# Kernel optimization log

Hardware: AMD Instinct MI355X
Metric: run time of the kernel (lower is better)

Reference implementation:

```python
import jax, jax.numpy as jnp
import numpy as np

B, N, NIN, NH, NOUT = 32, 64, 256, 256, 2
E = N * (N - 1)
BN_EPS = 1e-5


def _xavier(k, fan_in, fan_out):
    return jax.random.normal(k, (fan_in, fan_out), jnp.float32) * np.sqrt(2.0 / (fan_in + fan_out))


def _mlp_params(key, n_in, n_hid, n_out):
    k1, k2 = jax.random.split(key)
    return {
        'w1': _xavier(k1, n_in, n_hid), 'b1': jnp.full((n_hid,), 0.1, jnp.float32),
        'w2': _xavier(k2, n_hid, n_out), 'b2': jnp.full((n_out,), 0.1, jnp.float32),
        'g': jnp.ones((n_out,), jnp.float32), 'beta': jnp.zeros((n_out,), jnp.float32),
    }


def setup_inputs() -> dict:
    key = jax.random.key(0)
    ks = jax.random.split(key, 7)
    inputs = jax.random.normal(ks[0], (B, N, NIN), jnp.float32)
    # fully-connected directed graph w/o self loops: edge e = (send i, recv j), i != j
    idx = np.array([(i, j) for i in range(N) for j in range(N) if i != j], dtype=np.int64)
    rel_send = np.zeros((E, N), np.float32)
    rel_rec = np.zeros((E, N), np.float32)
    rel_send[np.arange(E), idx[:, 0]] = 1.0
    rel_rec[np.arange(E), idx[:, 1]] = 1.0
    out = {'inputs': inputs, 'rel_rec': jnp.asarray(rel_rec), 'rel_send': jnp.asarray(rel_send)}
    for name, (ni, nh, no), k in [('mlp1', (NIN, NH, NH), ks[1]),
                                  ('mlp2', (2 * NH, NH, NH), ks[2]),
                                  ('mlp3', (NH, NH, NH), ks[3]),
                                  ('mlp4', (3 * NH, NH, NH), ks[4])]:
        p = _mlp_params(k, ni, nh, no)
        for pk, pv in p.items():
            out[f'{name}_{pk}'] = pv
    out['fc_w'] = _xavier(ks[5], NH, NOUT)
    out['fc_b'] = jnp.full((NOUT,), 0.1, jnp.float32)
    return out


def _mlp(x, w1, b1, w2, b2, g, beta):
    # Linear -> ELU -> Linear -> ELU -> BatchNorm1d (training-mode batch stats, biased var)
    h = jax.nn.elu(x @ w1 + b1)
    h = jax.nn.elu(h @ w2 + b2)
    mean = h.mean(axis=(0, 1))
    var = h.var(axis=(0, 1))
    return (h - mean) * jax.lax.rsqrt(var + BN_EPS) * g + beta


def reference(inputs, rel_rec, rel_send,
              mlp1_w1, mlp1_b1, mlp1_w2, mlp1_b2, mlp1_g, mlp1_beta,
              mlp2_w1, mlp2_b1, mlp2_w2, mlp2_b2, mlp2_g, mlp2_beta,
              mlp3_w1, mlp3_b1, mlp3_w2, mlp3_b2, mlp3_g, mlp3_beta,
              mlp4_w1, mlp4_b1, mlp4_w2, mlp4_b2, mlp4_g, mlp4_beta,
              fc_w, fc_b):
    x = _mlp(inputs, mlp1_w1, mlp1_b1, mlp1_w2, mlp1_b2, mlp1_g, mlp1_beta)  # [B,N,NH]
    # node2edge: gather sender/receiver node features per edge
    s = jnp.einsum('en,bnh->beh', rel_send, x)
    r = jnp.einsum('en,bnh->beh', rel_rec, x)
    x = jnp.concatenate([s, r], axis=-1)  # [B,E,2*NH]
    x = _mlp(x, mlp2_w1, mlp2_b1, mlp2_w2, mlp2_b2, mlp2_g, mlp2_beta)
    x_skip = x
    # edge2node: scatter-sum incoming edges per node, normalized by N
    inc = jnp.einsum('en,beh->bnh', rel_rec, x) / N
    x = _mlp(inc, mlp3_w1, mlp3_b1, mlp3_w2, mlp3_b2, mlp3_g, mlp3_beta)
    s = jnp.einsum('en,bnh->beh', rel_send, x)
    r = jnp.einsum('en,bnh->beh', rel_rec, x)
    x = jnp.concatenate([s, r, x_skip], axis=-1)  # [B,E,3*NH]
    x = _mlp(x, mlp4_w1, mlp4_b1, mlp4_w2, mlp4_b2, mlp4_g, mlp4_beta)
    return x @ fc_w + fc_b  # [B,E,NOUT]
```

## Files before the change

### kernel.cpp

```cpp
#include <hip/hip_runtime.h>

typedef __bf16 bf16_t;
typedef __bf16 bf16x8 __attribute__((ext_vector_type(8)));
typedef float  f32x4  __attribute__((ext_vector_type(4)));

#define NB    64
#define EB    4032
#define BATCH 32
#define H     256
#define M_EDGE (BATCH*EB)
#define M_NODE (BATCH*NB)
#define T2    4
#define BN_EPS 1e-5f

__device__ __forceinline__ void load_lds16(const void* g, void* l) {
    __builtin_amdgcn_global_load_lds(
        (const __attribute__((address_space(1))) unsigned int*)g,
        (__attribute__((address_space(3))) unsigned int*)l, 16, 0, 0);
}
__device__ __forceinline__ float elu(float v) { return v > 0.f ? v : __expf(v) - 1.f; }

template<bool AF32>
__global__ __launch_bounds__(256)
void fused_mlp(const void* __restrict__ A0v,
               const bf16_t* __restrict__ W1t, const float* __restrict__ b1,
               const bf16_t* __restrict__ W2t, const float* __restrict__ b2,
               bf16_t* __restrict__ out, float* __restrict__ stats)
{
    const int m0 = blockIdx.x * 64;
    const int tid = threadIdx.x, wave = tid >> 6, lane = tid & 63;
    const int l15 = lane & 15, quad = lane >> 4;
    const int row = tid >> 2;
    const int cx8 = (((tid & 3) ^ ((tid >> 3) & 3))) * 8;
    const int sl8 = (tid & 3) * 8;
    const int xq8 = (quad ^ ((l15 >> 1) & 3)) * 8;

    __shared__ bf16_t h1s[64 * 264];
    __shared__ bf16_t Bs[256 * 32];
    __shared__ float  sred[512];

    const bf16_t* A0 = (const bf16_t*)A0v;

    f32x4 acc1[4][4];
#pragma unroll
    for (int t = 0; t < 4; ++t)
#pragma unroll
        for (int u = 0; u < 4; ++u) acc1[t][u] = (f32x4){0.f, 0.f, 0.f, 0.f};

    for (int k0 = 0; k0 < 256; k0 += 32) {
        bf16_t* ldsA = h1s + wave * 512;
        if (AF32) {
            const float* af = (const float*)A0v + (size_t)(m0 + row) * 256 + k0 + cx8;
            float4 lo = *(const float4*)af;
            float4 hi = *(const float4*)(af + 4);
            bf16x8 v;
            v[0]=(bf16_t)lo.x; v[1]=(bf16_t)lo.y; v[2]=(bf16_t)lo.z; v[3]=(bf16_t)lo.w;
            v[4]=(bf16_t)hi.x; v[5]=(bf16_t)hi.y; v[6]=(bf16_t)hi.z; v[7]=(bf16_t)hi.w;
            *(bf16x8*)&h1s[row * 32 + sl8] = v;
        } else {
            load_lds16(A0 + (size_t)(m0 + row) * 256 + k0 + cx8, ldsA);
        }
#pragma unroll
        for (int p = 0; p < 4; ++p)
            load_lds16(W1t + (size_t)(p * 64 + row) * 256 + k0 + cx8,
                       Bs + (p * 256 + wave * 64) * 8);
        __syncthreads();
        bf16x8 afr[4], bfr[4];
#pragma unroll
        for (int t = 0; t < 4; ++t)
            afr[t] = *(const bf16x8*)&h1s[(t * 16 + l15) * 32 + xq8];
#pragma unroll
        for (int u = 0; u < 4; ++u)
            bfr[u] = *(const bf16x8*)&Bs[(wave * 64 + u * 16 + l15) * 32 + xq8];
#pragma unroll
        for (int t = 0; t < 4; ++t)
#pragma unroll
            for (int u = 0; u < 4; ++u)
                acc1[t][u] = __builtin_amdgcn_mfma_f32_16x16x32_bf16(afr[t], bfr[u], acc1[t][u], 0, 0, 0);
        __syncthreads();
    }

#pragma unroll
    for (int u = 0; u < 4; ++u) {
        int   col = wave * 64 + u * 16 + l15;
        float bv  = b1[col];
#pragma unroll
        for (int t = 0; t < 4; ++t)
#pragma unroll
            for (int r = 0; r < 4; ++r)
                h1s[(t * 16 + quad * 4 + r) * 264 + col] = (bf16_t)elu(acc1[t][u][r] + bv);
    }
    sred[tid] = 0.f; sred[256 + tid] = 0.f;
    __syncthreads();

    f32x4 acc2[4][4];
#pragma unroll
    for (int t = 0; t < 4; ++t)
#pragma unroll
        for (int u = 0; u < 4; ++u) acc2[t][u] = (f32x4){0.f, 0.f, 0.f, 0.f};

    for (int k0 = 0; k0 < 256; k0 += 32) {
#pragma unroll
        for (int p = 0; p < 4; ++p)
            load_lds16(W2t + (size_t)(p * 64 + row) * 256 + k0 + cx8,
                       Bs + (p * 256 + wave * 64) * 8);
        __syncthreads();
        bf16x8 afr[4], bfr[4];
#pragma unroll
        for (int t = 0; t < 4; ++t)
            afr[t] = *(const bf16x8*)&h1s[(t * 16 + l15) * 264 + k0 + quad * 8];
#pragma unroll
        for (int u = 0; u < 4; ++u)
            bfr[u] = *(const bf16x8*)&Bs[(wave * 64 + u * 16 + l15) * 32 + xq8];
#pragma unroll
        for (int t = 0; t < 4; ++t)
#pragma unroll
            for (int u = 0; u < 4; ++u)
                acc2[t][u] = __builtin_amdgcn_mfma_f32_16x16x32_bf16(afr[t], bfr[u], acc2[t][u], 0, 0, 0);
        __syncthreads();
    }

#pragma unroll
    for (int u = 0; u < 4; ++u) {
        int   col = wave * 64 + u * 16 + l15;
        float bv  = b2[col];
        float s = 0.f, q = 0.f;
#pragma unroll
        for (int t = 0; t < 4; ++t)
#pragma unroll
            for (int r = 0; r < 4; ++r) {
                float v = elu(acc2[t][u][r] + bv);
                h1s[(t * 16 + quad * 4 + r) * 264 + col] = (bf16_t)v;
                s += v; q += v * v;
            }
        s += __shfl_xor(s, 16); s += __shfl_xor(s, 32);
        q += __shfl_xor(q, 16); q += __shfl_xor(q, 32);
        if (quad == 0) { atomicAdd(&sred[col], s); atomicAdd(&sred[256 + col], q); }
    }
    __syncthreads();
#pragma unroll
    for (int p = 0; p < 8; ++p) {
        int idx = p * 256 + tid;
        int r = idx >> 5, ch = idx & 31;
        *(uint4*)&out[(size_t)(m0 + r) * H + ch * 8] = *(const uint4*)&h1s[r * 264 + ch * 8];
    }
    atomicAdd(&stats[tid],     sred[tid]);
    atomicAdd(&stats[H + tid], sred[256 + tid]);
}

__global__ __launch_bounds__(256)
void node_gemm(const bf16_t* __restrict__ A, const float* __restrict__ statsIn,
               const float* __restrict__ g, const float* __restrict__ beta, float Mcnt,
               const bf16_t* __restrict__ Wt, const float* __restrict__ bias,
               float* __restrict__ out)
{
    const int m0 = blockIdx.x * 64;
    const int nb = blockIdx.y * 256;
    const int tid = threadIdx.x, wave = tid >> 6, lane = tid & 63;
    const int l15 = lane & 15, quad = lane >> 4;
    const int row = tid >> 2;
    const int cx8 = (((tid & 3) ^ ((tid >> 3) & 3))) * 8;
    const int sl8 = (tid & 3) * 8;
    const int xq8 = (quad ^ ((l15 >> 1) & 3)) * 8;
    __shared__ bf16_t As[64 * 32];
    __shared__ bf16_t Bs[256 * 32];
    __shared__ float  ss[512];

    {
        float mean = statsIn[tid] / Mcnt;
        float var  = statsIn[256 + tid] / Mcnt - mean * mean;
        float scl  = g[tid] * rsqrtf(var + BN_EPS);
        ss[tid]       = scl;
        ss[256 + tid] = beta[tid] - mean * scl;
    }
    __syncthreads();

    f32x4 acc[4][4];
#pragma unroll
    for (int t = 0; t < 4; ++t)
#pragma unroll
        for (int u = 0; u < 4; ++u) acc[t][u] = (f32x4){0.f, 0.f, 0.f, 0.f};

    for (int k0 = 0; k0 < 256; k0 += 32) {
        {
            int kc = k0 + cx8;
            bf16x8 v = *(const bf16x8*)(A + (size_t)(m0 + row) * 256 + kc);
            bf16x8 w;
#pragma unroll
            for (int j = 0; j < 8; ++j)
                w[j] = (bf16_t)((float)v[j] * ss[kc + j] + ss[256 + kc + j]);
            *(bf16x8*)&As[row * 32 + sl8] = w;
        }
#pragma unroll
        for (int p = 0; p < 4; ++p)
            load_lds16(Wt + (size_t)(nb + p * 64 + row) * 256 + k0 + cx8,
                       Bs + (p * 256 + wave * 64) * 8);
        __syncthreads();
        bf16x8 afr[4], bfr[4];
#pragma unroll
        for (int t = 0; t < 4; ++t)
            afr[t] = *(const bf16x8*)&As[(t * 16 + l15) * 32 + xq8];
#pragma unroll
        for (int u = 0; u < 4; ++u)
            bfr[u] = *(const bf16x8*)&Bs[(wave * 64 + u * 16 + l15) * 32 + xq8];
#pragma unroll
        for (int t = 0; t < 4; ++t)
#pragma unroll
            for (int u = 0; u < 4; ++u)
                acc[t][u] = __builtin_amdgcn_mfma_f32_16x16x32_bf16(afr[t], bfr[u], acc[t][u], 0, 0, 0);
        __syncthreads();
    }
#pragma unroll
    for (int u = 0; u < 4; ++u) {
        int col = nb + wave * 64 + u * 16 + l15;
        float bv = bias[col];
#pragma unroll
        for (int t = 0; t < 4; ++t)
#pragma unroll
            for (int r = 0; r < 4; ++r)
                out[(size_t)(m0 + t * 16 + quad * 4 + r) * 512 + col] = acc[t][u][r] + bv;
    }
}

__global__ __launch_bounds__(256, 2)
void m2_kernel(const float* __restrict__ PQ, const bf16_t* __restrict__ W2t,
               const float* __restrict__ b2, bf16_t* __restrict__ out,
               float* __restrict__ stats)
{
    const int tile0 = blockIdx.x * T2;
    const int tid = threadIdx.x, wave = tid >> 6, lane = tid & 63;
    const int l15 = lane & 15, quad = lane >> 4;

    __shared__ bf16_t Abuf[2][64 * 264];
    __shared__ float  sred[512];

    bf16x8 Breg[32];
#pragma unroll
    for (int ks = 0; ks < 8; ++ks)
#pragma unroll
        for (int u = 0; u < 4; ++u) {
            int col = wave * 64 + u * 16 + l15;
            Breg[ks * 4 + u] = *(const bf16x8*)(W2t + (size_t)col * 256 + ks * 32 + quad * 8);
        }
    sred[tid] = 0.f; sred[256 + tid] = 0.f;

    auto computeA = [&](int t, int b) {
        int row = tid >> 2;
        int m = (tile0 + t) * 64 + row;
        int bb = m / EB, e = m - bb * EB;
        int sn = e / (NB - 1), rr = e - sn * (NB - 1);
        int rc = rr + (rr >= sn ? 1 : 0);
        const float* Prow = PQ + (size_t)(bb * NB + sn) * 512;
        const float* Qrow = PQ + (size_t)(bb * NB + rc) * 512 + 256;
        int c0 = (tid & 3) * 64;
#pragma unroll
        for (int j = 0; j < 8; ++j) {
            int c = c0 + j * 8;
            float4 p0 = *(const float4*)(Prow + c);
            float4 p1 = *(const float4*)(Prow + c + 4);
            float4 q0 = *(const float4*)(Qrow + c);
            float4 q1 = *(const float4*)(Qrow + c + 4);
            bf16x8 v;
            v[0]=(bf16_t)elu(p0.x+q0.x); v[1]=(bf16_t)elu(p0.y+q0.y);
            v[2]=(bf16_t)elu(p0.z+q0.z); v[3]=(bf16_t)elu(p0.w+q0.w);
            v[4]=(bf16_t)elu(p1.x+q1.x); v[5]=(bf16_t)elu(p1.y+q1.y);
            v[6]=(bf16_t)elu(p1.z+q1.z); v[7]=(bf16_t)elu(p1.w+q1.w);
            *(bf16x8*)&Abuf[b][row * 264 + c] = v;
        }
    };

    computeA(0, 0);
    __syncthreads();

    for (int t = 0; t < T2; ++t) {
        const int cur = t & 1, nxt = cur ^ 1;
        if (t + 1 < T2) computeA(t + 1, nxt);

        f32x4 acc[4][4];
#pragma unroll
        for (int a = 0; a < 4; ++a)
#pragma unroll
            for (int u = 0; u < 4; ++u) acc[a][u] = (f32x4){0.f, 0.f, 0.f, 0.f};
#pragma unroll
        for (int ks = 0; ks < 8; ++ks) {
            bf16x8 afr[4];
#pragma unroll
            for (int a = 0; a < 4; ++a)
                afr[a] = *(const bf16x8*)&Abuf[cur][(a * 16 + l15) * 264 + ks * 32 + quad * 8];
#pragma unroll
            for (int a = 0; a < 4; ++a)
#pragma unroll
                for (int u = 0; u < 4; ++u)
                    acc[a][u] = __builtin_amdgcn_mfma_f32_16x16x32_bf16(afr[a], Breg[ks * 4 + u], acc[a][u], 0, 0, 0);
        }
        __syncthreads();

#pragma unroll
        for (int u = 0; u < 4; ++u) {
            int   col = wave * 64 + u * 16 + l15;
            float bv  = b2[col];
            float s = 0.f, q = 0.f;
#pragma unroll
            for (int a = 0; a < 4; ++a)
#pragma unroll
                for (int r = 0; r < 4; ++r) {
                    float v = elu(acc[a][u][r] + bv);
                    Abuf[cur][(a * 16 + quad * 4 + r) * 264 + col] = (bf16_t)v;
                    s += v; q += v * v;
                }
            s += __shfl_xor(s, 16); s += __shfl_xor(s, 32);
            q += __shfl_xor(q, 16); q += __shfl_xor(q, 32);
            if (quad == 0) { atomicAdd(&sred[col], s); atomicAdd(&sred[256 + col], q); }
        }
        __syncthreads();

        size_t m0 = (size_t)(tile0 + t) * 64;
#pragma unroll
        for (int p = 0; p < 8; ++p) {
            int idx = p * 256 + tid;
            int r = idx >> 5, ch = idx & 31;
            *(uint4*)&out[(m0 + r) * H + ch * 8] = *(const uint4*)&Abuf[cur][r * 264 + ch * 8];
        }
        __syncthreads();
    }
    atomicAdd(&stats[tid],     sred[tid]);
    atomicAdd(&stats[H + tid], sred[256 + tid]);
}

__global__ __launch_bounds__(256, 3)
void m4_kernel(const bf16_t* __restrict__ h2, const bf16_t* __restrict__ Wskf,
               const float* __restrict__ RS, const bf16_t* __restrict__ W4f,
               const float* __restrict__ b2, bf16_t* __restrict__ out,
               float* __restrict__ stats)
{
    const int m0 = blockIdx.x * 64;
    const int tid = threadIdx.x, wave = tid >> 6, lane = tid & 63;
    const int l15 = lane & 15, quad = lane >> 4;
    const int row = tid >> 2;
    const int c0 = (tid & 3) * 64;

    __shared__ bf16_t h1s[64 * 264];
    __shared__ float  sred[512];

    sred[tid] = 0.f; sred[256 + tid] = 0.f;

    {
        const bf16_t* src = h2 + (size_t)(m0 + row) * 256;
#pragma unroll
        for (int j = 0; j < 8; ++j) {
            int c = c0 + j * 8;
            *(bf16x8*)&h1s[row * 264 + c] = *(const bf16x8*)(src + c);
        }
    }

    const bf16_t* WskW = Wskf + (size_t)wave * 16384;
    const bf16_t* W4W  = W4f  + (size_t)wave * 16384;

    bf16x8 bcur[4], bnxt[4];
#pragma unroll
    for (int u = 0; u < 4; ++u)
        bcur[u] = *(const bf16x8*)(WskW + u * 512 + lane * 8);
    __syncthreads();

    f32x4 acc[4][4];
#pragma unroll
    for (int a = 0; a < 4; ++a)
#pragma unroll
        for (int u = 0; u < 4; ++u) acc[a][u] = (f32x4){0.f, 0.f, 0.f, 0.f};

#pragma unroll
    for (int ks = 0; ks < 8; ++ks) {
        if (ks < 7) {
#pragma unroll
            for (int u = 0; u < 4; ++u)
                bnxt[u] = *(const bf16x8*)(WskW + (ks + 1) * 2048 + u * 512 + lane * 8);
        }
        bf16x8 afr[4];
#pragma unroll
        for (int a = 0; a < 4; ++a)
            afr[a] = *(const bf16x8*)&h1s[(a * 16 + l15) * 264 + ks * 32 + quad * 8];
#pragma unroll
        for (int a = 0; a < 4; ++a)
#pragma unroll
            for (int u = 0; u < 4; ++u)
                acc[a][u] = __builtin_amdgcn_mfma_f32_16x16x32_bf16(afr[a], bcur[u], acc[a][u], 0, 0, 0);
#pragma unroll
        for (int u = 0; u < 4; ++u) bcur[u] = bnxt[u];
    }

#pragma unroll
    for (int u = 0; u < 4; ++u)
        bcur[u] = *(const bf16x8*)(W4W + u * 512 + lane * 8);
    __syncthreads();

#pragma unroll
    for (int u = 0; u < 4; ++u) {
        int col = wave * 64 + u * 16 + l15;
#pragma unroll
        for (int a = 0; a < 4; ++a)
#pragma unroll
            for (int r = 0; r < 4; ++r)
                h1s[(a * 16 + quad * 4 + r) * 264 + col] = (bf16_t)acc[a][u][r];
    }
    __syncthreads();

    {
        int m = m0 + row;
        int bb = m / EB, e = m - bb * EB;
        int sn = e / (NB - 1), rr = e - sn * (NB - 1);
        int rc = rr + (rr >= sn ? 1 : 0);
        const float* Srow = RS + (size_t)(bb * NB + sn) * 512;
        const float* Rrow = RS + (size_t)(bb * NB + rc) * 512 + 256;
#pragma unroll
        for (int j = 0; j < 8; ++j) {
            int c = c0 + j * 8;
            bf16x8 h = *(const bf16x8*)&h1s[row * 264 + c];
            float4 s0 = *(const float4*)(Srow + c);
            float4 s1 = *(const float4*)(Srow + c + 4);
            float4 r0 = *(const float4*)(Rrow + c);
            float4 r1 = *(const float4*)(Rrow + c + 4);
            bf16x8 v;
            v[0]=(bf16_t)elu((float)h[0]+s0.x+r0.x); v[1]=(bf16_t)elu((float)h[1]+s0.y+r0.y);
            v[2]=(bf16_t)elu((float)h[2]+s0.z+r0.z); v[3]=(bf16_t)elu((float)h[3]+s0.w+r0.w);
            v[4]=(bf16_t)elu((float)h[4]+s1.x+r1.x); v[5]=(bf16_t)elu((float)h[5]+s1.y+r1.y);
            v[6]=(bf16_t)elu((float)h[6]+s1.z+r1.z); v[7]=(bf16_t)elu((float)h[7]+s1.w+r1.w);
            *(bf16x8*)&h1s[row * 264 + c] = v;
        }
    }
    __syncthreads();

#pragma unroll
    for (int a = 0; a < 4; ++a)
#pragma unroll
        for (int u = 0; u < 4; ++u) acc[a][u] = (f32x4){0.f, 0.f, 0.f, 0.f};
#pragma unroll
    for (int ks = 0; ks < 8; ++ks) {
        if (ks < 7) {
#pragma unroll
            for (int u = 0; u < 4; ++u)
                bnxt[u] = *(const bf16x8*)(W4W + (ks + 1) * 2048 + u * 512 + lane * 8);
        }
        bf16x8 afr[4];
#pragma unroll
        for (int a = 0; a < 4; ++a)
            afr[a] = *(const bf16x8*)&h1s[(a * 16 + l15) * 264 + ks * 32 + quad * 8];
#pragma unroll
        for (int a = 0; a < 4; ++a)
#pragma unroll
            for (int u = 0; u < 4; ++u)
                acc[a][u] = __builtin_amdgcn_mfma_f32_16x16x32_bf16(afr[a], bcur[u], acc[a][u], 0, 0, 0);
#pragma unroll
        for (int u = 0; u < 4; ++u) bcur[u] = bnxt[u];
    }
    __syncthreads();

#pragma unroll
    for (int u = 0; u < 4; ++u) {
        int   col = wave * 64 + u * 16 + l15;
        float bv  = b2[col];
        float s = 0.f, q = 0.f;
#pragma unroll
        for (int a = 0; a < 4; ++a)
#pragma unroll
            for (int r = 0; r < 4; ++r) {
                float v = elu(acc[a][u][r] + bv);
                h1s[(a * 16 + quad * 4 + r) * 264 + col] = (bf16_t)v;
                s += v; q += v * v;
            }
        s += __shfl_xor(s, 16); s += __shfl_xor(s, 32);
        q += __shfl_xor(q, 16); q += __shfl_xor(q, 32);
        if (quad == 0) { atomicAdd(&sred[col], s); atomicAdd(&sred[256 + col], q); }
    }
    __syncthreads();

#pragma unroll
    for (int p = 0; p < 8; ++p) {
        int idx = p * 256 + tid;
        int r = idx >> 5, ch = idx & 31;
        *(uint4*)&out[(size_t)(m0 + r) * H + ch * 8] = *(const uint4*)&h1s[r * 264 + ch * 8];
    }
    atomicAdd(&stats[tid],     sred[tid]);
    atomicAdd(&stats[H + tid], sred[256 + tid]);
}

__global__ void prep(const float* __restrict__ w1a, bf16_t* __restrict__ wt1a,
                     const float* __restrict__ w1b, bf16_t* __restrict__ wt1b,
                     const float* __restrict__ w2b, bf16_t* __restrict__ wt2b,
                     const float* __restrict__ w3a, bf16_t* __restrict__ wt3a,
                     const float* __restrict__ w3b, bf16_t* __restrict__ wt3b,
                     const float* __restrict__ w4b, bf16_t* __restrict__ wt4b,
                     const float* __restrict__ w2a, bf16_t* __restrict__ wtpq,
                     const float* __restrict__ w4a, bf16_t* __restrict__ wtrs,
                     const float* __restrict__ b2a, float* __restrict__ biasPQ,
                     float* __restrict__ stats)
{
    int blk = blockIdx.x, tid = threadIdx.x;
    if (blk < 1536) {
        int grp = blk >> 8, lb = blk & 255;
        int idx = lb * 256 + tid;
        int k = idx >> 8, n = idx & 255;
        if (grp == 5) {
            int wv = n >> 6, u = (n >> 4) & 3, l15 = n & 15;
            int ks = k >> 5, qd = (k >> 3) & 3, j = k & 7;
            wt4b[wv * 16384 + ks * 2048 + u * 512 + (qd * 16 + l15) * 8 + j] = (bf16_t)w4b[idx];
        } else {
            const float* w; bf16_t* wt;
            switch (grp) {
                case 0: w = w1a; wt = wt1a; break;
                case 1: w = w1b; wt = wt1b; break;
                case 2: w = w2b; wt = wt2b; break;
                case 3: w = w3a; wt = wt3a; break;
                default: w = w3b; wt = wt3b; break;
            }
            wt[n * 256 + k] = (bf16_t)w[idx];
        }
    } else if (blk < 2560) {
        int lb = blk - 1536;
        const float* w = (lb < 512) ? w2a : w4a;
        bf16_t* wt = (lb < 512) ? wtpq : wtrs;
        int c = lb & 511, k = tid;
        float v = (c < 256) ? w[k * 256 + c] : w[(256 + k) * 256 + (c - 256)];
        wt[c * 256 + k] = (bf16_t)v;
    } else if (blk == 2560) {
        biasPQ[tid] = b2a[tid];
        biasPQ[256 + tid] = 0.f;
    } else {
        for (int j = 0; j < 8; ++j) stats[j * 256 + tid] = 0.f;
    }
}

__global__ void prep2(const float* __restrict__ w4a, const float* __restrict__ stats2,
                      const float* __restrict__ g2, const float* __restrict__ be2,
                      const float* __restrict__ b4a, bf16_t* __restrict__ wt,
                      float* __restrict__ bias)
{
    __shared__ float sh2s[256];
    int blk = blockIdx.x, tid = threadIdx.x;
    float mean = stats2[tid] / (float)M_EDGE;
    float var  = stats2[256 + tid] / (float)M_EDGE - mean * mean;
    float scl  = g2[tid] * rsqrtf(var + BN_EPS);
    if (blk < 256) {
        int n = blk, k = tid;
        int wv = n >> 6, u = (n >> 4) & 3, l15 = n & 15;
        int ks = k >> 5, qd = (k >> 3) & 3, j = k & 7;
        wt[wv * 16384 + ks * 2048 + u * 512 + (qd * 16 + l15) * 8 + j] =
            (bf16_t)(w4a[(512 + tid) * 256 + blk] * scl);
    } else {
        sh2s[tid] = be2[tid] - mean * scl;
        __syncthreads();
        float acc = 0.f;
        for (int k = 0; k < 256; ++k)
            acc += sh2s[k] * w4a[(512 + k) * 256 + tid];
        bias[tid] = b4a[tid] + acc;
        bias[256 + tid] = 0.f;
    }
}

__global__ void edge2node(const bf16_t* __restrict__ x2, const float* __restrict__ stats2,
                          const float* __restrict__ g2, const float* __restrict__ be2,
                          bf16_t* __restrict__ inc)
{
    int bn = blockIdx.x, bb = bn >> 6, n = bn & 63;
    int g = threadIdx.x >> 5, t = threadIdx.x & 31;
    __shared__ float part[8][256];
    __shared__ float ss[512];
    {
        int c = threadIdx.x;
        float mean = stats2[c] / (float)M_EDGE;
        float var  = stats2[256 + c] / (float)M_EDGE - mean * mean;
        float scl  = g2[c] * rsqrtf(var + BN_EPS);
        ss[c]       = scl;
        ss[256 + c] = be2[c] - mean * scl;
    }
    const bf16_t* base = x2 + (size_t)bb * EB * H;
    float a[8] = {0.f,0.f,0.f,0.f,0.f,0.f,0.f,0.f};
    for (int i = g; i < NB; i += 8) {
        if (i == n) continue;
        int e = i * (NB - 1) + n - (n > i ? 1 : 0);
        bf16x8 v = *(const bf16x8*)&base[(size_t)e * H + t * 8];
#pragma unroll
        for (int j = 0; j < 8; ++j) a[j] += (float)v[j];
    }
#pragma unroll
    for (int j = 0; j < 8; ++j) part[g][t * 8 + j] = a[j];
    __syncthreads();
    int c = threadIdx.x;
    float s = 0.f;
#pragma unroll
    for (int g2i = 0; g2i < 8; ++g2i) s += part[g2i][c];
    inc[(size_t)bn * H + c] = (bf16_t)(s * (1.f / 64.f) * ss[c] + ss[256 + c] * (63.f / 64.f));
}

__global__ void fc_kernel(const bf16_t* __restrict__ x4, const float* __restrict__ stats4,
                          const float* __restrict__ g4, const float* __restrict__ be4,
                          const float* __restrict__ fcw, const float* __restrict__ fcb,
                          float* __restrict__ out)
{
    __shared__ float ss[512];
    {
        int c = threadIdx.x;
        float mean = stats4[c] / (float)M_EDGE;
        float var  = stats4[256 + c] / (float)M_EDGE - mean * mean;
        float scl  = g4[c] * rsqrtf(var + BN_EPS);
        ss[c]       = scl;
        ss[256 + c] = be4[c] - mean * scl;
    }
    __syncthreads();
    int row  = blockIdx.x * 8 + (threadIdx.x >> 5);
    int t    = threadIdx.x & 31;
    bf16x8 v8 = *(const bf16x8*)(x4 + (size_t)row * H + t * 8);
    float s0 = 0.f, s1 = 0.f;
#pragma unroll
    for (int j = 0; j < 8; ++j) {
        int c = t * 8 + j;
        float v = (float)v8[j] * ss[c] + ss[256 + c];
        s0 += v * fcw[c * 2];
        s1 += v * fcw[c * 2 + 1];
    }
#pragma unroll
    for (int off = 16; off; off >>= 1) {
        s0 += __shfl_down(s0, off, 32);
        s1 += __shfl_down(s1, off, 32);
    }
    if (t == 0) {
        out[(size_t)row * 2]     = s0 + fcb[0];
        out[(size_t)row * 2 + 1] = s1 + fcb[1];
    }
}

extern "C" void kernel_launch(void* const* d_in, const int* in_sizes, int n_in,
                              void* d_out, int out_size, void* d_ws, size_t ws_size,
                              hipStream_t stream)
{
    (void)in_sizes; (void)n_in; (void)out_size; (void)ws_size;
    const float* inp = (const float*)d_in[0];
    const float* w1a = (const float*)d_in[3];  const float* b1a = (const float*)d_in[4];
    const float* w1b = (const float*)d_in[5];  const float* b1b = (const float*)d_in[6];
    const float* g1  = (const float*)d_in[7];  const float* be1 = (const float*)d_in[8];
    const float* w2a = (const float*)d_in[9];  const float* b2a = (const float*)d_in[10];
    const float* w2b = (const float*)d_in[11]; const float* b2b = (const float*)d_in[12];
    const float* g2  = (const float*)d_in[13]; const float* be2 = (const float*)d_in[14];
    const float* w3a = (const float*)d_in[15]; const float* b3a = (const float*)d_in[16];
    const float* w3b = (const float*)d_in[17]; const float* b3b = (const float*)d_in[18];
    const float* g3  = (const float*)d_in[19]; const float* be3 = (const float*)d_in[20];
    const float* w4a = (const float*)d_in[21]; const float* b4a = (const float*)d_in[22];
    const float* w4b = (const float*)d_in[23]; const float* b4b = (const float*)d_in[24];
    const float* g4  = (const float*)d_in[25]; const float* be4 = (const float*)d_in[26];
    const float* fcw = (const float*)d_in[27]; const float* fcb = (const float*)d_in[28];

    char* p = (char*)d_ws;
    auto alloc = [&](size_t nbytes) { char* r = p; p += (nbytes + 255) & ~(size_t)255; return r; };

    bf16_t* wt1a = (bf16_t*)alloc(256 * 256 * 2);
    bf16_t* wt1b = (bf16_t*)alloc(256 * 256 * 2);
    bf16_t* wt2b = (bf16_t*)alloc(256 * 256 * 2);
    bf16_t* wt3a = (bf16_t*)alloc(256 * 256 * 2);
    bf16_t* wt3b = (bf16_t*)alloc(256 * 256 * 2);
    bf16_t* wt4b = (bf16_t*)alloc(256 * 256 * 2);
    bf16_t* wtpq = (bf16_t*)alloc(512 * 256 * 2);
    bf16_t* wtrs = (bf16_t*)alloc(512 * 256 * 2);
    bf16_t* wtsk = (bf16_t*)alloc(256 * 256 * 2);
    float*  biasPQ = (float*)alloc(512 * sizeof(float));
    float*  biasRS = (float*)alloc(512 * sizeof(float));
    float*  stats  = (float*)alloc(4 * 512 * sizeof(float));
    bf16_t* x1   = (bf16_t*)alloc((size_t)M_NODE * H * 2);
    bf16_t* incb = (bf16_t*)alloc((size_t)M_NODE * H * 2);
    bf16_t* x3   = (bf16_t*)alloc((size_t)M_NODE * H * 2);
    float*  PQ   = (float*)alloc((size_t)M_NODE * 512 * sizeof(float));
    float*  RS   = (float*)alloc((size_t)M_NODE * 512 * sizeof(float));
    bf16_t* h2   = (bf16_t*)alloc((size_t)M_EDGE * H * 2);
    bf16_t* h4   = (bf16_t*)alloc((size_t)M_EDGE * H * 2);

    prep<<<2562, 256, 0, stream>>>(w1a, wt1a, w1b, wt1b, w2b, wt2b, w3a, wt3a,
                                   w3b, wt3b, w4b, wt4b, w2a, wtpq, w4a, wtrs,
                                   b2a, biasPQ, stats);

    fused_mlp<true ><<<M_NODE / 64, 256, 0, stream>>>(inp, wt1a, b1a, wt1b, b1b, x1, stats + 0);

    { dim3 g(M_NODE / 64, 2);
      node_gemm<<<g, 256, 0, stream>>>(x1, stats + 0, g1, be1, (float)M_NODE, wtpq, biasPQ, PQ); }

    m2_kernel<<<M_EDGE / (64 * T2), 256, 0, stream>>>(PQ, wt2b, b2b, h2, stats + 512);

    edge2node<<<M_NODE, 256, 0, stream>>>(h2, stats + 512, g2, be2, incb);
    fused_mlp<false><<<M_NODE / 64, 256, 0, stream>>>(incb, wt3a, b3a, wt3b, b3b, x3, stats + 1024);

    prep2<<<257, 256, 0, stream>>>(w4a, stats + 512, g2, be2, b4a, wtsk, biasRS);
    { dim3 g(M_NODE / 64, 2);
      node_gemm<<<g, 256, 0, stream>>>(x3, stats + 1024, g3, be3, (float)M_NODE, wtrs, biasRS, RS); }

    m4_kernel<<<M_EDGE / 64, 256, 0, stream>>>(h2, wtsk, RS, wt4b, b4b, h4, stats + 1536);

    fc_kernel<<<M_EDGE / 8, 256, 0, stream>>>(h4, stats + 1536, g4, be4, fcw, fcb, (float*)d_out);
}
```

Before: 372.1 us.

## Make m4_kernel persistent over four tiles with double-buffered A prefetch

```diff
diff --git a/kernel.cpp b/kernel.cpp
--- a/kernel.cpp
+++ b/kernel.cpp
@@ -11,6 +11,7 @@
 #define M_EDGE (BATCH*EB)
 #define M_NODE (BATCH*NB)
 #define T2    4
+#define T4    4
 #define BN_EPS 1e-5f
 
 __device__ __forceinline__ void load_lds16(const void* g, void* l) {
@@ -327,157 +328,172 @@
     atomicAdd(&stats[H + tid], sred[256 + tid]);
 }
 
-__global__ __launch_bounds__(256, 3)
+__global__ __launch_bounds__(256, 2)
 void m4_kernel(const bf16_t* __restrict__ h2, const bf16_t* __restrict__ Wskf,
                const float* __restrict__ RS, const bf16_t* __restrict__ W4f,
                const float* __restrict__ b2, bf16_t* __restrict__ out,
                float* __restrict__ stats)
 {
-    const int m0 = blockIdx.x * 64;
+    const int tile0 = blockIdx.x * T4;
     const int tid = threadIdx.x, wave = tid >> 6, lane = tid & 63;
     const int l15 = lane & 15, quad = lane >> 4;
     const int row = tid >> 2;
     const int c0 = (tid & 3) * 64;
 
-    __shared__ bf16_t h1s[64 * 264];
+    __shared__ bf16_t Abuf[2][64 * 264];
     __shared__ float  sred[512];
 
     sred[tid] = 0.f; sred[256 + tid] = 0.f;
-
-    {
-        const bf16_t* src = h2 + (size_t)(m0 + row) * 256;
-#pragma unroll
-        for (int j = 0; j < 8; ++j) {
-            int c = c0 + j * 8;
-            *(bf16x8*)&h1s[row * 264 + c] = *(const bf16x8*)(src + c);
-        }
-    }
 
     const bf16_t* WskW = Wskf + (size_t)wave * 16384;
     const bf16_t* W4W  = W4f  + (size_t)wave * 16384;
 
-    bf16x8 bcur[4], bnxt[4];
-#pragma unroll
-    for (int u = 0; u < 4; ++u)
-        bcur[u] = *(const bf16x8*)(WskW + u * 512 + lane * 8);
+    bf16x8 sreg[8];
+    auto loadA = [&](int t) {
+        const bf16_t* src = h2 + ((size_t)(tile0 + t) * 64 + row) * 256;
+#pragma unroll
+        for (int j = 0; j < 8; ++j)
+            sreg[j] = *(const bf16x8*)(src + c0 + j * 8);
+    };
+    auto writeA = [&](int b) {
+#pragma unroll
+        for (int j = 0; j < 8; ++j)
+            *(bf16x8*)&Abuf[b][row * 264 + c0 + j * 8] = sreg[j];
+    };
+
+    loadA(0); writeA(0);
     __syncthreads();
 
-    f32x4 acc[4][4];
-#pragma unroll
-    for (int a = 0; a < 4; ++a)
-#pragma unroll
-        for (int u = 0; u < 4; ++u) acc[a][u] = (f32x4){0.f, 0.f, 0.f, 0.f};
-
-#pragma unroll
-    for (int ks = 0; ks < 8; ++ks) {
-        if (ks < 7) {
-#pragma unroll
-            for (int u = 0; u < 4; ++u)
-                bnxt[u] = *(const bf16x8*)(WskW + (ks + 1) * 2048 + u * 512 + lane * 8);
-        }
-        bf16x8 afr[4];
+    for (int t = 0; t < T4; ++t) {
+        const int cur = t & 1, nxt = cur ^ 1;
+        if (t + 1 < T4) loadA(t + 1);
+
+        bf16x8 bcur[4], bnxt[4];
+#pragma unroll
+        for (int u = 0; u < 4; ++u)
+            bcur[u] = *(const bf16x8*)(WskW + u * 512 + lane * 8);
+
+        f32x4 acc[4][4];
 #pragma unroll
         for (int a = 0; a < 4; ++a)
-            afr[a] = *(const bf16x8*)&h1s[(a * 16 + l15) * 264 + ks * 32 + quad * 8];
+#pragma unroll
+            for (int u = 0; u < 4; ++u) acc[a][u] = (f32x4){0.f, 0.f, 0.f, 0.f};
+
+#pragma unroll
+        for (int ks = 0; ks < 8; ++ks) {
+            if (ks < 7) {
+#pragma unroll
+                for (int u = 0; u < 4; ++u)
+                    bnxt[u] = *(const bf16x8*)(WskW + (ks + 1) * 2048 + u * 512 + lane * 8);
+            }
+            bf16x8 afr[4];
+#pragma unroll
+            for (int a = 0; a < 4; ++a)
+                afr[a] = *(const bf16x8*)&Abuf[cur][(a * 16 + l15) * 264 + ks * 32 + quad * 8];
+#pragma unroll
+            for (int a = 0; a < 4; ++a)
+#pragma unroll
+                for (int u = 0; u < 4; ++u)
+                    acc[a][u] = __builtin_amdgcn_mfma_f32_16x16x32_bf16(afr[a], bcur[u], acc[a][u], 0, 0, 0);
+#pragma unroll
+            for (int u = 0; u < 4; ++u) bcur[u] = bnxt[u];
+        }
+
+#pragma unroll
+        for (int u = 0; u < 4; ++u)
+            bcur[u] = *(const bf16x8*)(W4W + u * 512 + lane * 8);
+
+        if (t + 1 < T4) writeA(nxt);
+        __syncthreads();
+
+#pragma unroll
+        for (int u = 0; u < 4; ++u) {
+            int col = wave * 64 + u * 16 + l15;
+#pragma unroll
+            for (int a = 0; a < 4; ++a)
+#pragma unroll
+                for (int r = 0; r < 4; ++r)
+                    Abuf[cur][(a * 16 + quad * 4 + r) * 264 + col] = (bf16_t)acc[a][u][r];
+        }
+        __syncthreads();
+
+        {
+            int m = (tile0 + t) * 64 + row;
+            int bb = m / EB, e = m - bb * EB;
+            int sn = e / (NB - 1), rr = e - sn * (NB - 1);
+            int rc = rr + (rr >= sn ? 1 : 0);
+            const float* Srow = RS + (size_t)(bb * NB + sn) * 512;
+            const float* Rrow = RS + (size_t)(bb * NB + rc) * 512 + 256;
+#pragma unroll
+            for (int j = 0; j < 8; ++j) {
+                int c = c0 + j * 8;
+                bf16x8 h = *(const bf16x8*)&Abuf[cur][row * 264 + c];
+                float4 s0 = *(const float4*)(Srow + c);
+                float4 s1 = *(const float4*)(Srow + c + 4);
+                float4 r0 = *(const float4*)(Rrow + c);
+                float4 r1 = *(const float4*)(Rrow + c + 4);
+                bf16x8 v;
+                v[0]=(bf16_t)elu((float)h[0]+s0.x+r0.x); v[1]=(bf16_t)elu((float)h[1]+s0.y+r0.y);
+                v[2]=(bf16_t)elu((float)h[2]+s0.z+r0.z); v[3]=(bf16_t)elu((float)h[3]+s0.w+r0.w);
+                v[4]=(bf16_t)elu((float)h[4]+s1.x+r1.x); v[5]=(bf16_t)elu((float)h[5]+s1.y+r1.y);
+                v[6]=(bf16_t)elu((float)h[6]+s1.z+r1.z); v[7]=(bf16_t)elu((float)h[7]+s1.w+r1.w);
+                *(bf16x8*)&Abuf[cur][row * 264 + c] = v;
+            }
+        }
+        __syncthreads();
+
 #pragma unroll
         for (int a = 0; a < 4; ++a)
 #pragma unroll
-            for (int u = 0; u < 4; ++u)
-                acc[a][u] = __builtin_amdgcn_mfma_f32_16x16x32_bf16(afr[a], bcur[u], acc[a][u], 0, 0, 0);
-#pragma unroll
-        for (int u = 0; u < 4; ++u) bcur[u] = bnxt[u];
-    }
-
-#pragma unroll
-    for (int u = 0; u < 4; ++u)
-        bcur[u] = *(const bf16x8*)(W4W + u * 512 + lane * 8);
-    __syncthreads();
-
-#pragma unroll
-    for (int u = 0; u < 4; ++u) {
-        int col = wave * 64 + u * 16 + l15;
-#pragma unroll
-        for (int a = 0; a < 4; ++a)
-#pragma unroll
-            for (int r = 0; r < 4; ++r)
-                h1s[(a * 16 + quad * 4 + r) * 264 + col] = (bf16_t)acc[a][u][r];
-    }
-    __syncthreads();
-
-    {
-        int m = m0 + row;
-        int bb = m / EB, e = m - bb * EB;
-        int sn = e / (NB - 1), rr = e - sn * (NB - 1);
-        int rc = rr + (rr >= sn ? 1 : 0);
-        const float* Srow = RS + (size_t)(bb * NB + sn) * 512;
-        const float* Rrow = RS + (size_t)(bb * NB + rc) * 512 + 256;
-#pragma unroll
-        for (int j = 0; j < 8; ++j) {
-            int c = c0 + j * 8;
-            bf16x8 h = *(const bf16x8*)&h1s[row * 264 + c];
-            float4 s0 = *(const float4*)(Srow + c);
-            float4 s1 = *(const float4*)(Srow + c + 4);
-            float4 r0 = *(const float4*)(Rrow + c);
-            float4 r1 = *(const float4*)(Rrow + c + 4);
-            bf16x8 v;
-            v[0]=(bf16_t)elu((float)h[0]+s0.x+r0.x); v[1]=(bf16_t)elu((float)h[1]+s0.y+r0.y);
-            v[2]=(bf16_t)elu((float)h[2]+s0.z+r0.z); v[3]=(bf16_t)elu((float)h[3]+s0.w+r0.w);
-            v[4]=(bf16_t)elu((float)h[4]+s1.x+r1.x); v[5]=(bf16_t)elu((float)h[5]+s1.y+r1.y);
-            v[6]=(bf16_t)elu((float)h[6]+s1.z+r1.z); v[7]=(bf16_t)elu((float)h[7]+s1.w+r1.w);
-            *(bf16x8*)&h1s[row * 264 + c] = v;
-        }
-    }
-    __syncthreads();
-
-#pragma unroll
-    for (int a = 0; a < 4; ++a)
-#pragma unroll
-        for (int u = 0; u < 4; ++u) acc[a][u] = (f32x4){0.f, 0.f, 0.f, 0.f};
-#pragma unroll
-    for (int ks = 0; ks < 8; ++ks) {
-        if (ks < 7) {
-#pragma unroll
-            for (int u = 0; u < 4; ++u)
-                bnxt[u] = *(const bf16x8*)(W4W + (ks + 1) * 2048 + u * 512 + lane * 8);
-        }
-        bf16x8 afr[4];
-#pragma unroll
-        for (int a = 0; a < 4; ++a)
-            afr[a] = *(const bf16x8*)&h1s[(a * 16 + l15) * 264 + ks * 32 + quad * 8];
-#pragma unroll
-        for (int a = 0; a < 4; ++a)
-#pragma unroll
-            for (int u = 0; u < 4; ++u)
-                acc[a][u] = __builtin_amdgcn_mfma_f32_16x16x32_bf16(afr[a], bcur[u], acc[a][u], 0, 0, 0);
-#pragma unroll
-        for (int u = 0; u < 4; ++u) bcur[u] = bnxt[u];
-    }
-    __syncthreads();
-
-#pragma unroll
-    for (int u = 0; u < 4; ++u) {
-        int   col = wave * 64 + u * 16 + l15;
-        float bv  = b2[col];
-        float s = 0.f, q = 0.f;
-#pragma unroll
-        for (int a = 0; a < 4; ++a)
-#pragma unroll
-            for (int r = 0; r < 4; ++r) {
-                float v = elu(acc[a][u][r] + bv);
-                h1s[(a * 16 + quad * 4 + r) * 264 + col] = (bf16_t)v;
-                s += v; q += v * v;
+            for (int u = 0; u < 4; ++u) acc[a][u] = (f32x4){0.f, 0.f, 0.f, 0.f};
+#pragma unroll
+        for (int ks = 0; ks < 8; ++ks) {
+            if (ks < 7) {
+#pragma unroll
+                for (int u = 0; u < 4; ++u)
+                    bnxt[u] = *(const bf16x8*)(W4W + (ks + 1) * 2048 + u * 512 + lane * 8);
             }
-        s += __shfl_xor(s, 16); s += __shfl_xor(s, 32);
-        q += __shfl_xor(q, 16); q += __shfl_xor(q, 32);
-        if (quad == 0) { atomicAdd(&sred[col], s); atomicAdd(&sred[256 + col], q); }
-    }
-    __syncthreads();
-
-#pragma unroll
-    for (int p = 0; p < 8; ++p) {
-        int idx = p * 256 + tid;
-        int r = idx >> 5, ch = idx & 31;
-        *(uint4*)&out[(size_t)(m0 + r) * H + ch * 8] = *(const uint4*)&h1s[r * 264 + ch * 8];
+            bf16x8 afr[4];
+#pragma unroll
+            for (int a = 0; a < 4; ++a)
+                afr[a] = *(const bf16x8*)&Abuf[cur][(a * 16 + l15) * 264 + ks * 32 + quad * 8];
+#pragma unroll
+            for (int a = 0; a < 4; ++a)
+#pragma unroll
+                for (int u = 0; u < 4; ++u)
+                    acc[a][u] = __builtin_amdgcn_mfma_f32_16x16x32_bf16(afr[a], bcur[u], acc[a][u], 0, 0, 0);
+#pragma unroll
+            for (int u = 0; u < 4; ++u) bcur[u] = bnxt[u];
+        }
+        __syncthreads();
+
+#pragma unroll
+        for (int u = 0; u < 4; ++u) {
+            int   col = wave * 64 + u * 16 + l15;
+            float bv  = b2[col];
+            float s = 0.f, q = 0.f;
+#pragma unroll
+            for (int a = 0; a < 4; ++a)
+#pragma unroll
+                for (int r = 0; r < 4; ++r) {
+                    float v = elu(acc[a][u][r] + bv);
+                    Abuf[cur][(a * 16 + quad * 4 + r) * 264 + col] = (bf16_t)v;
+                    s += v; q += v * v;
+                }
+            s += __shfl_xor(s, 16); s += __shfl_xor(s, 32);
+            q += __shfl_xor(q, 16); q += __shfl_xor(q, 32);
+            if (quad == 0) { atomicAdd(&sred[col], s); atomicAdd(&sred[256 + col], q); }
+        }
+        __syncthreads();
+
+        size_t m0 = (size_t)(tile0 + t) * 64;
+#pragma unroll
+        for (int p = 0; p < 8; ++p) {
+            int idx = p * 256 + tid;
+            int r = idx >> 5, ch = idx & 31;
+            *(uint4*)&out[(m0 + r) * H + ch * 8] = *(const uint4*)&Abuf[cur][r * 264 + ch * 8];
+        }
+        __syncthreads();
     }
     atomicAdd(&stats[tid],     sred[tid]);
     atomicAdd(&stats[H + tid], sred[256 + tid]);
@@ -689,7 +705,7 @@
     { dim3 g(M_NODE / 64, 2);
       node_gemm<<<g, 256, 0, stream>>>(x3, stats + 1024, g3, be3, (float)M_NODE, wtrs, biasRS, RS); }
 
-    m4_kernel<<<M_EDGE / 64, 256, 0, stream>>>(h2, wtsk, RS, wt4b, b4b, h4, stats + 1536);
+    m4_kernel<<<M_EDGE / (64 * T4), 256, 0, stream>>>(h2, wtsk, RS, wt4b, b4b, h4, stats + 1536);
 
     fc_kernel<<<M_EDGE / 8, 256, 0, stream>>>(h4, stats + 1536, g4, be4, fcw, fcb, (float*)d_out);
 }
```

Result: slower. 422.8 us (+13.6%).

## Load fused MLP weights directly into registers from pre-swizzled fragment layout

Applied to the files above, without the earlier changes.

```diff
diff --git a/kernel.cpp b/kernel.cpp
--- a/kernel.cpp
+++ b/kernel.cpp
@@ -21,104 +21,117 @@
 __device__ __forceinline__ float elu(float v) { return v > 0.f ? v : __expf(v) - 1.f; }
 
 template<bool AF32>
-__global__ __launch_bounds__(256)
+__global__ __launch_bounds__(256, 3)
 void fused_mlp(const void* __restrict__ A0v,
-               const bf16_t* __restrict__ W1t, const float* __restrict__ b1,
-               const bf16_t* __restrict__ W2t, const float* __restrict__ b2,
+               const bf16_t* __restrict__ W1f, const float* __restrict__ b1,
+               const bf16_t* __restrict__ W2f, const float* __restrict__ b2,
                bf16_t* __restrict__ out, float* __restrict__ stats)
 {
     const int m0 = blockIdx.x * 64;
     const int tid = threadIdx.x, wave = tid >> 6, lane = tid & 63;
     const int l15 = lane & 15, quad = lane >> 4;
     const int row = tid >> 2;
-    const int cx8 = (((tid & 3) ^ ((tid >> 3) & 3))) * 8;
-    const int sl8 = (tid & 3) * 8;
-    const int xq8 = (quad ^ ((l15 >> 1) & 3)) * 8;
+    const int c0 = (tid & 3) * 64;
 
     __shared__ bf16_t h1s[64 * 264];
-    __shared__ bf16_t Bs[256 * 32];
     __shared__ float  sred[512];
 
-    const bf16_t* A0 = (const bf16_t*)A0v;
-
-    f32x4 acc1[4][4];
-#pragma unroll
-    for (int t = 0; t < 4; ++t)
-#pragma unroll
-        for (int u = 0; u < 4; ++u) acc1[t][u] = (f32x4){0.f, 0.f, 0.f, 0.f};
-
-    for (int k0 = 0; k0 < 256; k0 += 32) {
-        bf16_t* ldsA = h1s + wave * 512;
-        if (AF32) {
-            const float* af = (const float*)A0v + (size_t)(m0 + row) * 256 + k0 + cx8;
-            float4 lo = *(const float4*)af;
-            float4 hi = *(const float4*)(af + 4);
+    sred[tid] = 0.f; sred[256 + tid] = 0.f;
+
+    if (AF32) {
+        const float* af = (const float*)A0v + (size_t)(m0 + row) * 256 + c0;
+#pragma unroll
+        for (int j = 0; j < 8; ++j) {
+            float4 lo = *(const float4*)(af + j * 8);
+            float4 hi = *(const float4*)(af + j * 8 + 4);
             bf16x8 v;
             v[0]=(bf16_t)lo.x; v[1]=(bf16_t)lo.y; v[2]=(bf16_t)lo.z; v[3]=(bf16_t)lo.w;
             v[4]=(bf16_t)hi.x; v[5]=(bf16_t)hi.y; v[6]=(bf16_t)hi.z; v[7]=(bf16_t)hi.w;
-            *(bf16x8*)&h1s[row * 32 + sl8] = v;
-        } else {
-            load_lds16(A0 + (size_t)(m0 + row) * 256 + k0 + cx8, ldsA);
-        }
-#pragma unroll
-        for (int p = 0; p < 4; ++p)
-            load_lds16(W1t + (size_t)(p * 64 + row) * 256 + k0 + cx8,
-                       Bs + (p * 256 + wave * 64) * 8);
-        __syncthreads();
-        bf16x8 afr[4], bfr[4];
-#pragma unroll
-        for (int t = 0; t < 4; ++t)
-            afr[t] = *(const bf16x8*)&h1s[(t * 16 + l15) * 32 + xq8];
-#pragma unroll
-        for (int u = 0; u < 4; ++u)
-            bfr[u] = *(const bf16x8*)&Bs[(wave * 64 + u * 16 + l15) * 32 + xq8];
-#pragma unroll
-        for (int t = 0; t < 4; ++t)
-#pragma unroll
-            for (int u = 0; u < 4; ++u)
-                acc1[t][u] = __builtin_amdgcn_mfma_f32_16x16x32_bf16(afr[t], bfr[u], acc1[t][u], 0, 0, 0);
-        __syncthreads();
-    }
+            *(bf16x8*)&h1s[row * 264 + c0 + j * 8] = v;
+        }
+    } else {
+        const bf16_t* src = (const bf16_t*)A0v + (size_t)(m0 + row) * 256 + c0;
+#pragma unroll
+        for (int j = 0; j < 8; ++j)
+            *(bf16x8*)&h1s[row * 264 + c0 + j * 8] = *(const bf16x8*)(src + j * 8);
+    }
+
+    const bf16_t* W1W = W1f + (size_t)wave * 16384;
+    const bf16_t* W2W = W2f + (size_t)wave * 16384;
+
+    bf16x8 bcur[4], bnxt[4];
+#pragma unroll
+    for (int u = 0; u < 4; ++u)
+        bcur[u] = *(const bf16x8*)(W1W + u * 512 + lane * 8);
+    __syncthreads();
+
+    f32x4 acc[4][4];
+#pragma unroll
+    for (int a = 0; a < 4; ++a)
+#pragma unroll
+        for (int u = 0; u < 4; ++u) acc[a][u] = (f32x4){0.f, 0.f, 0.f, 0.f};
+
+#pragma unroll
+    for (int ks = 0; ks < 8; ++ks) {
+        if (ks < 7) {
+#pragma unroll
+            for (int u = 0; u < 4; ++u)
+                bnxt[u] = *(const bf16x8*)(W1W + (ks + 1) * 2048 + u * 512 + lane * 8);
+        }
+        bf16x8 afr[4];
+#pragma unroll
+        for (int a = 0; a < 4; ++a)
+            afr[a] = *(const bf16x8*)&h1s[(a * 16 + l15) * 264 + ks * 32 + quad * 8];
+#pragma unroll
+        for (int a = 0; a < 4; ++a)
+#pragma unroll
+            for (int u = 0; u < 4; ++u)
+                acc[a][u] = __builtin_amdgcn_mfma_f32_16x16x32_bf16(afr[a], bcur[u], acc[a][u], 0, 0, 0);
+#pragma unroll
+        for (int u = 0; u < 4; ++u) bcur[u] = bnxt[u];
+    }
+
+#pragma unroll
+    for (int u = 0; u < 4; ++u)
+        bcur[u] = *(const bf16x8*)(W2W + u * 512 + lane * 8);
+    __syncthreads();
 
 #pragma unroll
     for (int u = 0; u < 4; ++u) {
         int   col = wave * 64 + u * 16 + l15;
         float bv  = b1[col];
 #pragma unroll
-        for (int t = 0; t < 4; ++t)
+        for (int a = 0; a < 4; ++a)
 #pragma unroll
             for (int r = 0; r < 4; ++r)
-                h1s[(t * 16 + quad * 4 + r) * 264 + col] = (bf16_t)elu(acc1[t][u][r] + bv);
-    }
-    sred[tid] = 0.f; sred[256 + tid] = 0.f;
-    __syncthreads();
-
-    f32x4 acc2[4][4];
-#pragma unroll
-    for (int t = 0; t < 4; ++t)
-#pragma unroll
-        for (int u = 0; u < 4; ++u) acc2[t][u] = (f32x4){0.f, 0.f, 0.f, 0.f};
-
-    for (int k0 = 0; k0 < 256; k0 += 32) {
-#pragma unroll
-        for (int p = 0; p < 4; ++p)
-            load_lds16(W2t + (size_t)(p * 64 + row) * 256 + k0 + cx8,
-                       Bs + (p * 256 + wave * 64) * 8);
-        __syncthreads();
-        bf16x8 afr[4], bfr[4];
-#pragma unroll
-        for (int t = 0; t < 4; ++t)
-            afr[t] = *(const bf16x8*)&h1s[(t * 16 + l15) * 264 + k0 + quad * 8];
-#pragma unroll
-        for (int u = 0; u < 4; ++u)
-            bfr[u] = *(const bf16x8*)&Bs[(wave * 64 + u * 16 + l15) * 32 + xq8];
-#pragma unroll
-        for (int t = 0; t < 4; ++t)
-#pragma unroll
-            for (int u = 0; u < 4; ++u)
-                acc2[t][u] = __builtin_amdgcn_mfma_f32_16x16x32_bf16(afr[t], bfr[u], acc2[t][u], 0, 0, 0);
-        __syncthreads();
-    }
+                h1s[(a * 16 + quad * 4 + r) * 264 + col] = (bf16_t)elu(acc[a][u][r] + bv);
+    }
+    __syncthreads();
+
+#pragma unroll
+    for (int a = 0; a < 4; ++a)
+#pragma unroll
+        for (int u = 0; u < 4; ++u) acc[a][u] = (f32x4){0.f, 0.f, 0.f, 0.f};
+#pragma unroll
+    for (int ks = 0; ks < 8; ++ks) {
+        if (ks < 7) {
+#pragma unroll
+            for (int u = 0; u < 4; ++u)
+                bnxt[u] = *(const bf16x8*)(W2W + (ks + 1) * 2048 + u * 512 + lane * 8);
+        }
+        bf16x8 afr[4];
+#pragma unroll
+        for (int a = 0; a < 4; ++a)
+            afr[a] = *(const bf16x8*)&h1s[(a * 16 + l15) * 264 + ks * 32 + quad * 8];
+#pragma unroll
+        for (int a = 0; a < 4; ++a)
+#pragma unroll
+            for (int u = 0; u < 4; ++u)
+                acc[a][u] = __builtin_amdgcn_mfma_f32_16x16x32_bf16(afr[a], bcur[u], acc[a][u], 0, 0, 0);
+#pragma unroll
+        for (int u = 0; u < 4; ++u) bcur[u] = bnxt[u];
+    }
+    __syncthreads();
 
 #pragma unroll
     for (int u = 0; u < 4; ++u) {
@@ -126,11 +139,11 @@
         float bv  = b2[col];
         float s = 0.f, q = 0.f;
 #pragma unroll
-        for (int t = 0; t < 4; ++t)
+        for (int a = 0; a < 4; ++a)
 #pragma unroll
             for (int r = 0; r < 4; ++r) {
-                float v = elu(acc2[t][u][r] + bv);
-                h1s[(t * 16 + quad * 4 + r) * 264 + col] = (bf16_t)v;
+                float v = elu(acc[a][u][r] + bv);
+                h1s[(a * 16 + quad * 4 + r) * 264 + col] = (bf16_t)v;
                 s += v; q += v * v;
             }
         s += __shfl_xor(s, 16); s += __shfl_xor(s, 32);
@@ -138,6 +151,7 @@
         if (quad == 0) { atomicAdd(&sred[col], s); atomicAdd(&sred[256 + col], q); }
     }
     __syncthreads();
+
 #pragma unroll
     for (int p = 0; p < 8; ++p) {
         int idx = p * 256 + tid;
@@ -499,20 +513,20 @@
         int grp = blk >> 8, lb = blk & 255;
         int idx = lb * 256 + tid;
         int k = idx >> 8, n = idx & 255;
-        if (grp == 5) {
-            int wv = n >> 6, u = (n >> 4) & 3, l15 = n & 15;
-            int ks = k >> 5, qd = (k >> 3) & 3, j = k & 7;
-            wt4b[wv * 16384 + ks * 2048 + u * 512 + (qd * 16 + l15) * 8 + j] = (bf16_t)w4b[idx];
+        if (grp == 2) {
+            wt2b[n * 256 + k] = (bf16_t)w2b[idx];
         } else {
             const float* w; bf16_t* wt;
             switch (grp) {
                 case 0: w = w1a; wt = wt1a; break;
                 case 1: w = w1b; wt = wt1b; break;
-                case 2: w = w2b; wt = wt2b; break;
                 case 3: w = w3a; wt = wt3a; break;
-                default: w = w3b; wt = wt3b; break;
+                case 4: w = w3b; wt = wt3b; break;
+                default: w = w4b; wt = wt4b; break;
             }
-            wt[n * 256 + k] = (bf16_t)w[idx];
+            int wv = n >> 6, u = (n >> 4) & 3, l15 = n & 15;
+            int ks = k >> 5, qd = (k >> 3) & 3, j = k & 7;
+            wt[wv * 16384 + ks * 2048 + u * 512 + (qd * 16 + l15) * 8 + j] = (bf16_t)w[idx];
         }
     } else if (blk < 2560) {
         int lb = blk - 1536;
```

Result: faster. 362.4 us (-2.6%).
